# Kernel tuning notes

Hardware: AMD Instinct MI355X
Metric: run time of the kernel (lower is better)

The kernel has to match this reference:

```python
import jax, jax.numpy as jnp
import numpy as np

L, H, NH, FF = 12, 768, 12, 3072
HD = H // NH
B, T = 8, 512
SCALE = 1.0 / float(np.sqrt(HD))
EPS = 1e-12


def setup_inputs() -> dict:
    key = jax.random.key(0)
    ks = jax.random.split(key, 10)
    s = jnp.float32(0.02)

    def p(k, shape):
        return jax.random.normal(k, shape, dtype=jnp.float32) * s

    return {
        "hidden_states": jax.random.normal(ks[0], (B, T, H), dtype=jnp.float32),
        "attention_mask": jnp.ones((B, T), dtype=jnp.float32),
        "Wq": p(ks[1], (L, H, H)), "bq": jnp.zeros((L, H), jnp.float32),
        "Wk": p(ks[2], (L, H, H)), "bk": jnp.zeros((L, H), jnp.float32),
        "Wv": p(ks[3], (L, H, H)), "bv": jnp.zeros((L, H), jnp.float32),
        "Wao": p(ks[4], (L, H, H)), "bao": jnp.zeros((L, H), jnp.float32),
        "ln1_g": jnp.ones((L, H), jnp.float32), "ln1_b": jnp.zeros((L, H), jnp.float32),
        "Wi": p(ks[5], (L, H, FF)), "bi": jnp.zeros((L, FF), jnp.float32),
        "Wo": p(ks[6], (L, FF, H)), "bo": jnp.zeros((L, H), jnp.float32),
        "ln2_g": jnp.ones((L, H), jnp.float32), "ln2_b": jnp.zeros((L, H), jnp.float32),
    }


def _layernorm(x, g, b):
    m = jnp.mean(x, axis=-1, keepdims=True)
    v = jnp.mean((x - m) ** 2, axis=-1, keepdims=True)
    return (x - m) * jax.lax.rsqrt(v + EPS) * g + b


def _encoder(hidden_states, attention_mask, params):
    # additive mask: (1 - mask) * -10000, broadcast to [B, 1, 1, T]
    add_mask = (1.0 - attention_mask)[:, None, None, :] * -10000.0

    def layer(x, p):
        wq, bq, wk, bk, wv, bv, wao, bao, g1, b1, wi, bi, wo, bo, g2, b2 = p
        q = (x @ wq + bq).reshape(B, T, NH, HD)
        k = (x @ wk + bk).reshape(B, T, NH, HD)
        v = (x @ wv + bv).reshape(B, T, NH, HD)
        scores = jnp.einsum('bihd,bjhd->bhij', q, k) * SCALE + add_mask
        probs = jax.nn.softmax(scores, axis=-1)  # dropout p=0 (eval)
        ctx = jnp.einsum('bhij,bjhd->bihd', probs, v).reshape(B, T, H)
        attn_out = _layernorm(ctx @ wao + bao + x, g1, b1)
        ff = jax.nn.gelu(attn_out @ wi + bi, approximate=False)
        out = _layernorm(ff @ wo + bo + attn_out, g2, b2)
        return out, None

    out, _ = jax.lax.scan(layer, hidden_states, params)
    return out


def reference(hidden_states, attention_mask, Wq, bq, Wk, bk, Wv, bv, Wao, bao,
              ln1_g, ln1_b, Wi, bi, Wo, bo, ln2_g, ln2_b):
    params = (Wq, bq, Wk, bk, Wv, bv, Wao, bao, ln1_g, ln1_b, Wi, bi, Wo, bo, ln2_g, ln2_b)
    return _encoder(hidden_states, attention_mask, params)
```

## Files before the change

### kernel.cpp

```cpp
#include <hip/hip_runtime.h>
#include <hip/hip_bf16.h>

typedef __bf16 bf16;
typedef __attribute__((ext_vector_type(8))) __bf16 bf16x8;
typedef __attribute__((ext_vector_type(4))) float f32x4;

#define MFMA16(a, b, c) __builtin_amdgcn_mfma_f32_16x16x32_bf16((a), (b), (c), 0, 0, 0)

#define WAIT_VM(N) asm volatile("s_waitcnt vmcnt(" #N ")" ::: "memory")
#define BAR() do { __builtin_amdgcn_s_barrier(); __builtin_amdgcn_sched_barrier(0); } while (0)
#define SYNC_VM(N) do { WAIT_VM(N); BAR(); } while (0)
#define SYNC_LGKM() do { asm volatile("s_waitcnt lgkmcnt(0)" ::: "memory"); BAR(); } while (0)

__device__ __forceinline__ void async16(const bf16* g, bf16* l) {
    __builtin_amdgcn_global_load_lds((__attribute__((address_space(1))) void*)(g),
                                     (__attribute__((address_space(3))) void*)(l), 16, 0, 0);
}

__device__ __forceinline__ void xcd_swizzle(int& bx, int& by, int& bz) {
    const int gx = gridDim.x, gy = gridDim.y;
    const int nwg = gx * gy * gridDim.z;
    const int lin = blockIdx.x + gx * (blockIdx.y + gy * blockIdx.z);
    const int xcd = lin & 7, seq = lin >> 3;
    const int q = nwg >> 3, r = nwg & 7;
    const int nl = (xcd < r ? xcd * (q + 1) : r * (q + 1) + (xcd - r) * q) + seq;
    bx = nl % gx;
    const int t = nl / gx;
    by = t % gy;
    bz = t / gy;
}

template <int MODE, int BM>
__global__ __launch_bounds__(256) void gemm_kernel(
    const bf16* __restrict__ A, const bf16* __restrict__ WT,
    const float* __restrict__ b0, const float* __restrict__ b1, const float* __restrict__ b2,
    int s1, int s2,
    void* __restrict__ o0, void* __restrict__ o1,
    int N, int K, int Kpart)
{
    constexpr int MT = BM / 32;
    __shared__ __align__(16) bf16 sA[3][BM * 32];
    __shared__ __align__(16) bf16 sB[3][128 * 32];

    const int tid  = threadIdx.x;
    const int lane = tid & 63;
    const int wave = tid >> 6;
    const int quad = lane >> 4;
    const int l15  = lane & 15;
    const int wm   = (wave >> 1) * (BM / 2);
    const int wn   = (wave & 1) * 64;

    int bxs, bys, bzs;
    xcd_swizzle(bxs, bys, bzs);
    const int bm = bys * BM;
    const int bn = bxs * 128;
    const int kbase = bzs * Kpart;

    f32x4 acc[MT][4];
#pragma unroll
    for (int i = 0; i < MT; i++)
#pragma unroll
        for (int j = 0; j < 4; j++)
#pragma unroll
            for (int r = 0; r < 4; r++) acc[i][j][r] = 0.0f;

    const int idx1 = tid + 256;
    const int ra0 = tid >> 2,  ca0 = (((tid  & 3) ^ ((ra0 >> 1) & 3)) * 8);
    const int rb1 = idx1 >> 2, cb1 = (((idx1 & 3) ^ ((rb1 >> 1) & 3)) * 8);

    const bf16* Arow0 = A + (size_t)(bm + ra0) * K + kbase + ca0;
    const bf16* Arow1 = (BM == 128) ? A + (size_t)(bm + rb1) * K + kbase + cb1 : A;
    const bf16* Brow0 = WT + (size_t)(bn + ra0) * K + kbase + ca0;
    const bf16* Brow1 = WT + (size_t)(bn + rb1) * K + kbase + cb1;

    const int nk = Kpart >> 5;

    auto stage = [&](int kt, int buf) {
        const int ko = kt * 32;
        async16(Arow0 + ko, sA[buf] + tid * 8);
        if (BM == 128) async16(Arow1 + ko, sA[buf] + idx1 * 8);
        async16(Brow0 + ko, sB[buf] + tid * 8);
        async16(Brow1 + ko, sB[buf] + idx1 * 8);
    };

    stage(0, 0);
    if (nk > 1) stage(1, 1);
    if (nk > 2) stage(2, 2);

    const int chF = (quad ^ ((l15 >> 1) & 3)) * 8;

    int cur = 0;
    for (int kt = 0; kt < nk; kt++) {
        if (kt + 2 < nk) {
            if (BM == 128) { WAIT_VM(8); } else { WAIT_VM(6); }
        } else if (kt + 1 < nk) {
            if (BM == 128) { WAIT_VM(4); } else { WAIT_VM(3); }
        } else {
            WAIT_VM(0);
        }
        BAR();

        bf16x8 af[MT], bfr[4];
#pragma unroll
        for (int i = 0; i < MT; i++)
            af[i] = *(const bf16x8*)(sA[cur] + (wm + i * 16 + l15) * 32 + chF);
#pragma unroll
        for (int i = 0; i < 4; i++)
            bfr[i] = *(const bf16x8*)(sB[cur] + (wn + i * 16 + l15) * 32 + chF);
#pragma unroll
        for (int mt = 0; mt < MT; mt++)
#pragma unroll
            for (int nt = 0; nt < 4; nt++)
                acc[mt][nt] = MFMA16(af[mt], bfr[nt], acc[mt][nt]);

        SYNC_LGKM();
        if (kt + 3 < nk) stage(kt + 3, cur);
        cur = (cur == 2) ? 0 : cur + 1;
    }

    void* outp = (bzs == 0) ? o0 : o1;

#pragma unroll
    for (int nt = 0; nt < 4; nt++) {
        const int col = bn + wn + nt * 16 + l15;
        float bias = 0.0f;
        if (MODE != 1)
            bias = (col < s1) ? b0[col] : (col < s2) ? b1[col - s1] : b2[col - s2];
#pragma unroll
        for (int mt = 0; mt < MT; mt++) {
#pragma unroll
            for (int r = 0; r < 4; r++) {
                const int row = bm + wm + mt * 16 + quad * 4 + r;
                float v = acc[mt][nt][r] + bias;
                if (MODE == 2) v = 0.5f * v * (1.0f + erff(v * 0.70710678118654752f));
                if (MODE == 1) ((float*)outp)[(size_t)row * N + col] = v;
                else           ((bf16*)outp)[(size_t)row * N + col] = (bf16)v;
            }
        }
    }
}

__global__ __launch_bounds__(256) void vtrans_kernel(
    const bf16* __restrict__ qkv, bf16* __restrict__ vT)
{
    const int bh = blockIdx.y;
    const int b = bh / 12, h = bh - b * 12;
    const int k0 = blockIdx.x * 128;
    __shared__ __align__(16) bf16 tile[128 * 72];
    const int tid = threadIdx.x;
    const bf16* src = qkv + (size_t)(b * 512 + k0) * 2304 + 1536 + h * 64;
#pragma unroll
    for (int i = 0; i < 4; i++) {
        const int idx = i * 256 + tid;
        const int r = idx >> 3, c = (idx & 7) * 8;
        *(uint4*)(tile + r * 72 + c) = *(const uint4*)(src + (size_t)r * 2304 + c);
    }
    __syncthreads();
    bf16* dst = vT + (size_t)bh * 64 * 512 + k0;
#pragma unroll
    for (int i = 0; i < 4; i++) {
        const int idx = i * 256 + tid;
        const int d = idx & 63, kg = idx >> 6;
        alignas(16) bf16 tmp[8];
#pragma unroll
        for (int e = 0; e < 8; e++) tmp[e] = tile[(kg * 8 + e) * 72 + d];
        *(uint4*)(dst + (size_t)d * 512 + kg * 8) = *(uint4*)tmp;
    }
}

__global__ __launch_bounds__(256) void attn_kernel(
    const bf16* __restrict__ qkv, const bf16* __restrict__ vT,
    const float* __restrict__ mask, bf16* __restrict__ ctx)
{
    int bxs, bys, bzs;
    xcd_swizzle(bxs, bys, bzs);
    const int b = bzs, h = bys, q0 = bxs * 32;
    const int bh = b * 12 + h;
    const int tid = threadIdx.x, lane = tid & 63, wave = tid >> 6;
    const int quad = lane >> 4, l15 = lane & 15;
    const int mt = wave & 1;
    const int whi = wave >> 1;

    __shared__ __align__(16) bf16 sKV[2][64 * 64];
    __shared__ __align__(16) bf16 sS[32 * 520];
    __shared__ float sAM[512];
    __shared__ float sRed[256];
    __shared__ float sRow[32];

    for (int i = tid; i < 512; i += 256)
        sAM[i] = (1.0f - mask[b * 512 + i]) * -10000.0f;

    const size_t RS = 2304;
    const bf16* Qrow = qkv + (size_t)(b * 512 + q0 + mt * 16 + l15) * RS + h * 64;
    const bf16x8 aQ0 = *(const bf16x8*)(Qrow + quad * 8);
    const bf16x8 aQ1 = *(const bf16x8*)(Qrow + 32 + quad * 8);

    const int c0 = tid, c1 = tid + 256;
    const int r0 = c0 >> 3, r1 = c1 >> 3;
    const int sc0 = ((c0 & 7) ^ (r0 & 7)) * 8;
    const int sc1 = ((c1 & 7) ^ (r1 & 7)) * 8;

    const bf16* Kbase = qkv + (size_t)(b * 512) * RS + 768 + h * 64;

    async16(Kbase + (size_t)(r0) * RS + sc0, (bf16*)sKV[0] + c0 * 8);
    async16(Kbase + (size_t)(r1) * RS + sc1, (bf16*)sKV[0] + c1 * 8);

#pragma unroll
    for (int kt = 0; kt < 8; kt++) {
        const int cur = kt & 1;
        if (kt < 7) {
            async16(Kbase + (size_t)((kt + 1) * 64 + r0) * RS + sc0, (bf16*)sKV[cur ^ 1] + c0 * 8);
            async16(Kbase + (size_t)((kt + 1) * 64 + r1) * RS + sc1, (bf16*)sKV[cur ^ 1] + c1 * 8);
            SYNC_VM(2);
        } else {
            SYNC_VM(0);
        }
#pragma unroll
        for (int n = 0; n < 2; n++) {
            const int nt = whi * 2 + n;
            const int krow = nt * 16 + l15;
            const int sw = krow & 7;
            bf16x8 bK0 = *(const bf16x8*)(sKV[cur] + krow * 64 + ((quad ^ sw) * 8));
            bf16x8 bK1 = *(const bf16x8*)(sKV[cur] + krow * 64 + (((4 + quad) ^ sw) * 8));
            f32x4 accS;
#pragma unroll
            for (int r = 0; r < 4; r++) accS[r] = 0.0f;
            accS = MFMA16(aQ0, bK0, accS);
            accS = MFMA16(aQ1, bK1, accS);
#pragma unroll
            for (int r = 0; r < 4; r++) {
                const int row = mt * 16 + quad * 4 + r;
                sS[row * 520 + kt * 64 + nt * 16 + l15] = (bf16)accS[r];
            }
        }
        SYNC_LGKM();
    }

    const bf16* Vbase = vT + (size_t)bh * 64 * 512;
    async16(Vbase + (size_t)r0 * 512 + sc0, (bf16*)sKV[0] + c0 * 8);
    async16(Vbase + (size_t)r1 * 512 + sc1, (bf16*)sKV[0] + c1 * 8);

    {
        const int r = tid >> 3, p = tid & 7;
        float mx = -1e30f;
#pragma unroll
        for (int t = 0; t < 8; t++) {
            const int v0 = (p + 8 * t) * 8;
            bf16x8 pv = *(const bf16x8*)(sS + r * 520 + v0);
#pragma unroll
            for (int e = 0; e < 8; e++)
                mx = fmaxf(mx, (float)pv[e] * 0.125f + sAM[v0 + e]);
        }
        sRed[r * 8 + p] = mx;
        SYNC_LGKM();
#pragma unroll
        for (int q = 0; q < 8; q++) mx = fmaxf(mx, sRed[r * 8 + q]);
        float sum = 0.0f;
#pragma unroll
        for (int t = 0; t < 8; t++) {
            const int v0 = (p + 8 * t) * 8;
            bf16x8 pv = *(const bf16x8*)(sS + r * 520 + v0);
            bf16x8 ev;
#pragma unroll
            for (int e = 0; e < 8; e++) {
                const float x = __expf((float)pv[e] * 0.125f + sAM[v0 + e] - mx);
                sum += x;
                ev[e] = (bf16)x;
            }
            *(bf16x8*)(sS + r * 520 + v0) = ev;
        }
        SYNC_LGKM();
        sRed[r * 8 + p] = sum;
        SYNC_LGKM();
        if (p == 0) {
            float s = 0.0f;
#pragma unroll
            for (int q = 0; q < 8; q++) s += sRed[r * 8 + q];
            sRow[r] = s;
        }
    }

    f32x4 accO[2];
#pragma unroll
    for (int i = 0; i < 2; i++)
#pragma unroll
        for (int r = 0; r < 4; r++) accO[i][r] = 0.0f;

#pragma unroll
    for (int kt = 0; kt < 8; kt++) {
        const int cur = kt & 1;
        if (kt < 7) {
            async16(Vbase + (size_t)r0 * 512 + (kt + 1) * 64 + sc0, (bf16*)sKV[cur ^ 1] + c0 * 8);
            async16(Vbase + (size_t)r1 * 512 + (kt + 1) * 64 + sc1, (bf16*)sKV[cur ^ 1] + c1 * 8);
            SYNC_VM(2);
        } else {
            SYNC_VM(0);
        }
#pragma unroll
        for (int kk = 0; kk < 2; kk++) {
            bf16x8 aP = *(const bf16x8*)(sS + (mt * 16 + l15) * 520 + kt * 64 + kk * 32 + quad * 8);
#pragma unroll
            for (int n = 0; n < 2; n++) {
                const int vrow = whi * 32 + n * 16 + l15;
                bf16x8 bV = *(const bf16x8*)(sKV[cur] + vrow * 64 + (((kk * 4 + quad) ^ (vrow & 7)) * 8));
                accO[n] = MFMA16(aP, bV, accO[n]);
            }
        }
        SYNC_LGKM();
    }
#pragma unroll
    for (int n = 0; n < 2; n++) {
#pragma unroll
        for (int r = 0; r < 4; r++) {
            const int row = mt * 16 + quad * 4 + r;
            const float o = accO[n][r] / sRow[row];
            ctx[(size_t)(b * 512 + q0 + row) * 768 + h * 64 + whi * 32 + n * 16 + l15] = (bf16)o;
        }
    }
}

template <int NP>
__global__ __launch_bounds__(256) void ln_kernel(
    const float* __restrict__ p0, const float* __restrict__ p1,
    const float* __restrict__ bias, const float* __restrict__ resid,
    const float* __restrict__ g, const float* __restrict__ bb,
    bf16* __restrict__ out_bf, float* __restrict__ out_f32)
{
    const int row = blockIdx.x;
    const int tid = threadIdx.x;
    __shared__ float sS[4], sQ[4];

    float x[3], s = 0.0f, sq = 0.0f;
#pragma unroll
    for (int j = 0; j < 3; j++) {
        const int c = tid + j * 256;
        const size_t idx = (size_t)row * 768 + c;
        float v = p0[idx] + bias[c] + resid[idx];
        if (NP > 1) v += p1[idx];
        x[j] = v; s += v; sq += v * v;
    }
#pragma unroll
    for (int off = 32; off; off >>= 1) { s += __shfl_down(s, off); sq += __shfl_down(sq, off); }
    if ((tid & 63) == 0) { sS[tid >> 6] = s; sQ[tid >> 6] = sq; }
    __syncthreads();
    s  = sS[0] + sS[1] + sS[2] + sS[3];
    sq = sQ[0] + sQ[1] + sQ[2] + sQ[3];
    const float mean = s * (1.0f / 768.0f);
    float var = sq * (1.0f / 768.0f) - mean * mean;
    var = fmaxf(var, 0.0f);
    const float rstd = rsqrtf(var + 1e-12f);
#pragma unroll
    for (int j = 0; j < 3; j++) {
        const int c = tid + j * 256;
        const float v = (x[j] - mean) * rstd * g[c] + bb[c];
        out_bf[(size_t)row * 768 + c] = (bf16)v;
        out_f32[(size_t)row * 768 + c] = v;
    }
}

__global__ __launch_bounds__(256) void transpose_kernel(
    const float* __restrict__ Wq, const float* __restrict__ Wk, const float* __restrict__ Wv,
    const float* __restrict__ Wao, const float* __restrict__ Wi, const float* __restrict__ Wo,
    bf16* __restrict__ wT)
{
    __shared__ bf16 tile[64 * 68];
    int id = blockIdx.x;
    const float* src; bf16* dst; int Kd, Nd;
    if (id < 576) {
        const int w = id / 144; id -= w * 144;
        Kd = 768; Nd = 768;
        src = (w == 0) ? Wq : (w == 1) ? Wk : (w == 2) ? Wv : Wao;
        dst = wT + (size_t)w * 589824;
    } else if (id < 1152) {
        id -= 576; Kd = 768; Nd = 3072; src = Wi; dst = wT + 2359296;
    } else {
        id -= 1152; Kd = 3072; Nd = 768; src = Wo; dst = wT + 4718592;
    }
    const int tn = Nd >> 6;
    const int tr = id / tn, tc = id - tr * tn;
    const int r0 = tr * 64, c0 = tc * 64;
    const int tid = threadIdx.x;

#pragma unroll
    for (int i = 0; i < 4; i++) {
        const int idx = i * 256 + tid;
        const int r = idx >> 4, c4 = (idx & 15) * 4;
        const float4 f = *(const float4*)(src + (size_t)(r0 + r) * Nd + c0 + c4);
        alignas(8) bf16 q[4] = {(bf16)f.x, (bf16)f.y, (bf16)f.z, (bf16)f.w};
        *(ushort4*)(tile + r * 68 + c4) = *(ushort4*)q;
    }
    __syncthreads();
#pragma unroll
    for (int i = 0; i < 4; i++) {
        const int idx = i * 256 + tid;
        const int n = idx >> 4, kc = (idx & 15) * 4;
        alignas(8) bf16 tmp[4];
#pragma unroll
        for (int e = 0; e < 4; e++) tmp[e] = tile[(kc + e) * 68 + n];
        *(ushort4*)(dst + (size_t)(c0 + n) * Kd + r0 + kc) = *(ushort4*)tmp;
    }
}

__global__ __launch_bounds__(256) void convert_kernel(
    const float* __restrict__ in, bf16* __restrict__ out, int n)
{
    const int i = blockIdx.x * 256 + threadIdx.x;
    if (i < n) out[i] = (bf16)in[i];
}

extern "C" void kernel_launch(void* const* d_in, const int* in_sizes, int n_in,
                              void* d_out, int out_size, void* d_ws, size_t ws_size,
                              hipStream_t stream)
{
    const float* hidden = (const float*)d_in[0];
    const float* mask   = (const float*)d_in[1];
    const float* Wq  = (const float*)d_in[2];  const float* bq  = (const float*)d_in[3];
    const float* Wk  = (const float*)d_in[4];  const float* bk  = (const float*)d_in[5];
    const float* Wv  = (const float*)d_in[6];  const float* bv  = (const float*)d_in[7];
    const float* Wao = (const float*)d_in[8];  const float* bao = (const float*)d_in[9];
    const float* g1  = (const float*)d_in[10]; const float* be1 = (const float*)d_in[11];
    const float* Wi  = (const float*)d_in[12]; const float* bi  = (const float*)d_in[13];
    const float* Wo  = (const float*)d_in[14]; const float* bo  = (const float*)d_in[15];
    const float* g2  = (const float*)d_in[16]; const float* be2 = (const float*)d_in[17];

    char* ws = (char*)d_ws;
    bf16*  wT    = (bf16*)(ws);
    bf16*  qkv   = (bf16*)(ws + 14155776);
    bf16*  vT    = (bf16*)(ws + 33030144);
    bf16*  ctx   = (bf16*)(ws + 39321600);
    bf16*  attnb = (bf16*)(ws + 45613056);
    bf16*  xb    = (bf16*)(ws + 51904512);
    float* xf    = (float*)(ws + 58195968);
    float* attnf = (float*)(ws + 70778880);
    bf16*  ffh   = (bf16*)(ws + 14155776);
    float* pA0   = (float*)(ws + 14155776);
    float* pA1   = (float*)(ws + 26738688);
    float* pF0   = (float*)(ws + 39321600);
    float* pF1   = (float*)(ws + 83361792);

    convert_kernel<<<12288, 256, 0, stream>>>(hidden, xb, 3145728);

    for (int l = 0; l < 12; l++) {
        transpose_kernel<<<1728, 256, 0, stream>>>(
            Wq + (size_t)l * 589824, Wk + (size_t)l * 589824, Wv + (size_t)l * 589824,
            Wao + (size_t)l * 589824, Wi + (size_t)l * 2359296, Wo + (size_t)l * 2359296, wT);

        gemm_kernel<0, 64><<<dim3(18, 64, 1), 256, 0, stream>>>(
            xb, wT, bq + l * 768, bk + l * 768, bv + l * 768, 768, 1536,
            qkv, nullptr, 2304, 768, 768);

        vtrans_kernel<<<dim3(4, 96), 256, 0, stream>>>(qkv, vT);

        attn_kernel<<<dim3(16, 12, 8), 256, 0, stream>>>(qkv, vT, mask, ctx);

        gemm_kernel<1, 64><<<dim3(6, 64, 2), 256, 0, stream>>>(
            ctx, wT + 1769472, nullptr, nullptr, nullptr, 0, 0,
            pA0, pA1, 768, 768, 384);

        const float* resid1 = (l == 0) ? hidden : xf;
        ln_kernel<2><<<4096, 256, 0, stream>>>(
            pA0, pA1, bao + l * 768, resid1, g1 + l * 768, be1 + l * 768, attnb, attnf);

        gemm_kernel<2, 128><<<dim3(24, 32, 1), 256, 0, stream>>>(
            attnb, wT + 2359296, bi + l * 3072, bi + l * 3072, bi + l * 3072, 3072, 3072,
            ffh, nullptr, 3072, 768, 768);

        gemm_kernel<1, 64><<<dim3(6, 64, 2), 256, 0, stream>>>(
            ffh, wT + 4718592, nullptr, nullptr, nullptr, 0, 0,
            pF0, pF1, 768, 3072, 1536);

        float* f32dst = (l == 11) ? (float*)d_out : xf;
        ln_kernel<2><<<4096, 256, 0, stream>>>(
            pF0, pF1, bo + l * 768, attnf, g2 + l * 768, be2 + l * 768, xb, f32dst);
    }
}
```

Before: 2.550 ms.

## Enlarge GEMM tiles to 128x256 with 512 threads and double buffering

The GEMM kernel moves from 256-thread blocks with 64/128x128 tiles and a three-stage LDS pipeline to 512-thread blocks with a fixed 128x256 tile and a two-stage pipeline. Each wave now computes a 64x64 subtile, which raises operand reuse per LDS load and cuts global traffic per output. All four GEMM launches use the new grids. The cost is fewer blocks per GEMM (e.g. 288 for QKV, 192 for the projection GEMMs), which may underfill the 256 CUs, and a shallower prefetch depth that hides less memory latency.

```diff
diff --git a/kernel.cpp b/kernel.cpp
--- a/kernel.cpp
+++ b/kernel.cpp
@@ -30,92 +30,83 @@
     bz = t / gy;
 }
 
-template <int MODE, int BM>
-__global__ __launch_bounds__(256) void gemm_kernel(
+template <int MODE>
+__global__ __launch_bounds__(512) void gemm_kernel(
     const bf16* __restrict__ A, const bf16* __restrict__ WT,
     const float* __restrict__ b0, const float* __restrict__ b1, const float* __restrict__ b2,
     int s1, int s2,
     void* __restrict__ o0, void* __restrict__ o1,
     int N, int K, int Kpart)
 {
-    constexpr int MT = BM / 32;
-    __shared__ __align__(16) bf16 sA[3][BM * 32];
-    __shared__ __align__(16) bf16 sB[3][128 * 32];
+    __shared__ __align__(16) bf16 sA[2][128 * 32];
+    __shared__ __align__(16) bf16 sB[2][256 * 32];
 
     const int tid  = threadIdx.x;
     const int lane = tid & 63;
     const int wave = tid >> 6;
     const int quad = lane >> 4;
     const int l15  = lane & 15;
-    const int wm   = (wave >> 1) * (BM / 2);
-    const int wn   = (wave & 1) * 64;
+    const int wm   = (wave >> 2) * 64;
+    const int wn   = (wave & 3) * 64;
 
     int bxs, bys, bzs;
     xcd_swizzle(bxs, bys, bzs);
-    const int bm = bys * BM;
-    const int bn = bxs * 128;
+    const int bm = bys * 128;
+    const int bn = bxs * 256;
     const int kbase = bzs * Kpart;
 
-    f32x4 acc[MT][4];
-#pragma unroll
-    for (int i = 0; i < MT; i++)
+    f32x4 acc[4][4];
+#pragma unroll
+    for (int i = 0; i < 4; i++)
 #pragma unroll
         for (int j = 0; j < 4; j++)
 #pragma unroll
             for (int r = 0; r < 4; r++) acc[i][j][r] = 0.0f;
 
-    const int idx1 = tid + 256;
-    const int ra0 = tid >> 2,  ca0 = (((tid  & 3) ^ ((ra0 >> 1) & 3)) * 8);
-    const int rb1 = idx1 >> 2, cb1 = (((idx1 & 3) ^ ((rb1 >> 1) & 3)) * 8);
-
-    const bf16* Arow0 = A + (size_t)(bm + ra0) * K + kbase + ca0;
-    const bf16* Arow1 = (BM == 128) ? A + (size_t)(bm + rb1) * K + kbase + cb1 : A;
-    const bf16* Brow0 = WT + (size_t)(bn + ra0) * K + kbase + ca0;
-    const bf16* Brow1 = WT + (size_t)(bn + rb1) * K + kbase + cb1;
+    const int cA  = tid;
+    const int rA  = cA >> 2,  kA  = (((cA  & 3) ^ ((rA  >> 1) & 3)) * 8);
+    const int cB0 = tid;
+    const int rB0 = cB0 >> 2, kB0 = (((cB0 & 3) ^ ((rB0 >> 1) & 3)) * 8);
+    const int cB1 = tid + 512;
+    const int rB1 = cB1 >> 2, kB1 = (((cB1 & 3) ^ ((rB1 >> 1) & 3)) * 8);
+
+    const bf16* Arow  = A  + (size_t)(bm + rA)  * K + kbase + kA;
+    const bf16* Brow0 = WT + (size_t)(bn + rB0) * K + kbase + kB0;
+    const bf16* Brow1 = WT + (size_t)(bn + rB1) * K + kbase + kB1;
 
     const int nk = Kpart >> 5;
 
-    auto stage = [&](int kt, int buf) {
-        const int ko = kt * 32;
-        async16(Arow0 + ko, sA[buf] + tid * 8);
-        if (BM == 128) async16(Arow1 + ko, sA[buf] + idx1 * 8);
-        async16(Brow0 + ko, sB[buf] + tid * 8);
-        async16(Brow1 + ko, sB[buf] + idx1 * 8);
-    };
-
-    stage(0, 0);
-    if (nk > 1) stage(1, 1);
-    if (nk > 2) stage(2, 2);
+    async16(Arow,  sA[0] + cA  * 8);
+    async16(Brow0, sB[0] + cB0 * 8);
+    async16(Brow1, sB[0] + cB1 * 8);
 
     const int chF = (quad ^ ((l15 >> 1) & 3)) * 8;
 
     int cur = 0;
     for (int kt = 0; kt < nk; kt++) {
-        if (kt + 2 < nk) {
-            if (BM == 128) { WAIT_VM(8); } else { WAIT_VM(6); }
-        } else if (kt + 1 < nk) {
-            if (BM == 128) { WAIT_VM(4); } else { WAIT_VM(3); }
+        if (kt + 1 < nk) {
+            const int ko = (kt + 1) * 32;
+            async16(Arow  + ko, sA[cur ^ 1] + cA  * 8);
+            async16(Brow0 + ko, sB[cur ^ 1] + cB0 * 8);
+            async16(Brow1 + ko, sB[cur ^ 1] + cB1 * 8);
+            SYNC_VM(3);
         } else {
-            WAIT_VM(0);
-        }
-        BAR();
-
-        bf16x8 af[MT], bfr[4];
-#pragma unroll
-        for (int i = 0; i < MT; i++)
+            SYNC_VM(0);
+        }
+        bf16x8 af[4], bfr[4];
+#pragma unroll
+        for (int i = 0; i < 4; i++)
             af[i] = *(const bf16x8*)(sA[cur] + (wm + i * 16 + l15) * 32 + chF);
 #pragma unroll
         for (int i = 0; i < 4; i++)
             bfr[i] = *(const bf16x8*)(sB[cur] + (wn + i * 16 + l15) * 32 + chF);
 #pragma unroll
-        for (int mt = 0; mt < MT; mt++)
+        for (int mt = 0; mt < 4; mt++)
 #pragma unroll
             for (int nt = 0; nt < 4; nt++)
                 acc[mt][nt] = MFMA16(af[mt], bfr[nt], acc[mt][nt]);
-
-        SYNC_LGKM();
-        if (kt + 3 < nk) stage(kt + 3, cur);
-        cur = (cur == 2) ? 0 : cur + 1;
+        SYNC_LGKM();
+        cur ^= 1;
     }
 
     void* outp = (bzs == 0) ? o0 : o1;
@@ -127,7 +118,7 @@
         if (MODE != 1)
             bias = (col < s1) ? b0[col] : (col < s2) ? b1[col - s1] : b2[col - s2];
 #pragma unroll
-        for (int mt = 0; mt < MT; mt++) {
+        for (int mt = 0; mt < 4; mt++) {
 #pragma unroll
             for (int r = 0; r < 4; r++) {
                 const int row = bm + wm + mt * 16 + quad * 4 + r;
@@ -445,7 +436,7 @@
             Wq + (size_t)l * 589824, Wk + (size_t)l * 589824, Wv + (size_t)l * 589824,
             Wao + (size_t)l * 589824, Wi + (size_t)l * 2359296, Wo + (size_t)l * 2359296, wT);
 
-        gemm_kernel<0, 64><<<dim3(18, 64, 1), 256, 0, stream>>>(
+        gemm_kernel<0><<<dim3(9, 32, 1), 512, 0, stream>>>(
             xb, wT, bq + l * 768, bk + l * 768, bv + l * 768, 768, 1536,
             qkv, nullptr, 2304, 768, 768);
 
@@ -453,7 +444,7 @@
 
         attn_kernel<<<dim3(16, 12, 8), 256, 0, stream>>>(qkv, vT, mask, ctx);
 
-        gemm_kernel<1, 64><<<dim3(6, 64, 2), 256, 0, stream>>>(
+        gemm_kernel<1><<<dim3(3, 32, 2), 512, 0, stream>>>(
             ctx, wT + 1769472, nullptr, nullptr, nullptr, 0, 0,
             pA0, pA1, 768, 768, 384);
 
@@ -461,11 +452,11 @@
         ln_kernel<2><<<4096, 256, 0, stream>>>(
             pA0, pA1, bao + l * 768, resid1, g1 + l * 768, be1 + l * 768, attnb, attnf);
 
-        gemm_kernel<2, 128><<<dim3(24, 32, 1), 256, 0, stream>>>(
+        gemm_kernel<2><<<dim3(12, 32, 1), 512, 0, stream>>>(
             attnb, wT + 2359296, bi + l * 3072, bi + l * 3072, bi + l * 3072, 3072, 3072,
             ffh, nullptr, 3072, 768, 768);
 
-        gemm_kernel<1, 64><<<dim3(6, 64, 2), 256, 0, stream>>>(
+        gemm_kernel<1><<<dim3(3, 32, 2), 512, 0, stream>>>(
             ffh, wT + 4718592, nullptr, nullptr, nullptr, 0, 0,
             pF0, pF1, 768, 3072, 1536);
 
```

After: 2.548 ms. Within noise of the previous version (-0.1%).
